# Performance work log

Measured on AMD Instinct MI355X. Metric: run time of the kernel, lower is better.

Reference implementation:

```python
import jax, jax.numpy as jnp
import numpy as np

# dims: batch, num queries, context len, model dim, heads, head dim,
# num_q_group, v_repeat, lora rank
B, NQ, NC, D = 4, 416, 257, 768
H, DH = 6, 128
G, R, LORA = 104, 4, 64  # NQ == R * G, all_q_mid == G * LORA
EPS = 1e-5


def ln(x, g, b):
    m = jnp.mean(x, axis=-1, keepdims=True)
    v = jnp.mean(jnp.square(x - m), axis=-1, keepdims=True)
    return (x - m) * jax.lax.rsqrt(v + EPS) * g + b


def setup_inputs() -> dict:
    key = jax.random.key(0)
    ks = jax.random.split(key, 7)
    s = 0.02
    return {
        "x": jax.random.normal(ks[0], (B, NQ, D), dtype=jnp.float32),
        "context": jax.random.normal(ks[1], (B, NC, D), dtype=jnp.float32),
        "Wq": jax.random.normal(ks[2], (D, D), dtype=jnp.float32) * s,
        "gq": jnp.ones((D,), jnp.float32), "bq": jnp.zeros((D,), jnp.float32),
        "Wk": jax.random.normal(ks[3], (D, D), dtype=jnp.float32) * s,
        "gk": jnp.ones((D,), jnp.float32), "bk": jnp.zeros((D,), jnp.float32),
        "Wv": jax.random.normal(ks[4], (D, G * LORA), dtype=jnp.float32) * s,
        "gv1": jnp.ones((G * LORA,), jnp.float32), "bv1": jnp.zeros((G * LORA,), jnp.float32),
        "Wconv": jax.random.normal(ks[5], (G, LORA, D), dtype=jnp.float32) * s,  # grouped 1x1 conv: per-group (LORA -> D)
        "gv2": jnp.ones((D,), jnp.float32), "bv2": jnp.zeros((D,), jnp.float32),
        "Wo": jax.random.normal(ks[6], (D, D), dtype=jnp.float32) * s,
        "go": jnp.ones((D,), jnp.float32), "bo": jnp.zeros((D,), jnp.float32),
    }


def reference(x, context, Wq, gq, bq, Wk, gk, bk, Wv, gv1, bv1, Wconv, gv2, bv2, Wo, go, bo):
    # to_q / to_k: Linear (no bias) + affine LayerNorm
    q = ln(x @ Wq, gq, bq)          # (B, NQ, D)
    k = ln(context @ Wk, gk, bk)    # (B, NC, D)
    # split heads -> (B*H, n, DH)
    q = q.reshape(B, NQ, H, DH).transpose(0, 2, 1, 3).reshape(B * H, NQ, DH)
    k = k.reshape(B, NC, H, DH).transpose(0, 2, 1, 3).reshape(B * H, NC, DH)

    # q-aware to_v: Linear -> LN -> grouped 1x1 Conv1d -> LN, plus skip of context
    mid = ln(context @ Wv, gv1, bv1)                 # (B, NC, G*LORA)
    mid = mid.reshape(B, NC, G, LORA)
    v = jnp.einsum('bngl,gld->bgnd', mid, Wconv)     # grouped conv, (B, G, NC, D)
    v = ln(v, gv2, bv2)
    v = v + context[:, None]                          # v_has_skip: context.unsqueeze(1)
    # heads: (B, G, NC, H, DH) -> (B*H, G, NC, DH)
    v = v.reshape(B, G, NC, H, DH).transpose(0, 3, 1, 2, 4).reshape(B * H, G, NC, DH)

    scale = DH ** (-0.25)
    sim = jnp.einsum('bid,bjd->bij', q * scale, k * scale)   # (B*H, NQ, NC)
    attn = jax.nn.softmax(sim, axis=-1)                       # dropout in eval mode: identity

    # torch repeat(1, R, 1, 1) tiles v along q-dim: query i uses group i % G.
    # reshape attn to (B*H, R, G, NC) so that i = r*G + g maps to group g.
    attn_g = attn.reshape(B * H, R, G, NC)
    out = jnp.einsum('brgj,bgjd->brgd', attn_g, v).reshape(B * H, NQ, DH)

    # merge heads -> (B, NQ, D)
    out = out.reshape(B, H, NQ, DH).transpose(0, 2, 1, 3).reshape(B, NQ, D)
    # to_out: Linear (no bias) + Dropout(eval: identity) + affine LayerNorm
    return ln(out @ Wo, go, bo)
```

## Files before the change

kernel.cpp:

```cpp
#include <hip/hip_runtime.h>


typedef unsigned short u16;
typedef unsigned int   u32;
typedef __attribute__((ext_vector_type(4))) float f32x4;
typedef __attribute__((ext_vector_type(4))) u32   u32x4;
typedef __attribute__((ext_vector_type(8))) short bf16x8;

__device__ __forceinline__ float bf2f(u16 v) { return __uint_as_float(((u32)v) << 16); }
__device__ __forceinline__ u16 f2bf(float f) {
  u32 u = __float_as_uint(f);
  u32 r = u + 0x7fffu + ((u >> 16) & 1u);
  return (u16)(r >> 16);
}
__device__ __forceinline__ float gld(const void* p, long idx, int f32) {
  return f32 ? ((const float*)p)[idx] : bf2f(((const u16*)p)[idx]);
}

typedef const __attribute__((address_space(1))) u32 gas_u32;
typedef __attribute__((address_space(3))) u32 las_u32;

__device__ __forceinline__ void stage16(const u16* g, u16* lbase, int lane) {
#if __has_builtin(__builtin_amdgcn_global_load_lds)
  (void)lane;
  __builtin_amdgcn_global_load_lds((gas_u32*)g, (las_u32*)lbase, 16, 0, 0);
#else
  *(u32x4*)(lbase + lane * 8) = *(const u32x4*)g;
#endif
}

__global__ __launch_bounds__(256) void probe_k(const u32* __restrict__ xw, int* __restrict__ flag) {
  int tid = threadIdx.x, c = 0;
  for (int i = tid; i < 4096; i += 256) {
    u16 lo = (u16)(xw[i] & 0xffffu);
    float a = fabsf(bf2f(lo));
    if (lo == 0 || (a >= 1e-3f && a <= 32.f)) ++c;
  }
#pragma unroll
  for (int o = 32; o; o >>= 1) c += __shfl_xor(c, o, 64);
  __shared__ int r[4];
  if ((tid & 63) == 0) r[tid >> 6] = c;
  __syncthreads();
  if (tid == 0) flag[0] = (r[0] + r[1] + r[2] + r[3] >= 2048) ? 0 : 1;
}

__global__ __launch_bounds__(256) void fill_k(u16* p, float v, int n) {
  int i = blockIdx.x * 256 + threadIdx.x;
  if (i < n) p[i] = f2bf(v);
}

__global__ __launch_bounds__(256) void prep_k(
    const void* __restrict__ x,   u16* __restrict__ xb,
    const void* __restrict__ ctx, u16* __restrict__ cbuf,
    const void* __restrict__ Wcv, u16* __restrict__ wcvb,
    u16* __restrict__ midi,
    const void* __restrict__ Wq, const void* __restrict__ Wk,
    const void* __restrict__ Wo, const void* __restrict__ Wv,
    u16* __restrict__ wqt, u16* __restrict__ wkt, u16* __restrict__ wot,
    u16* __restrict__ wvt, u16* __restrict__ ctxT,
    float* __restrict__ wbar, const int* __restrict__ dtf)
{
  const int f = dtf[0];
  int bid = blockIdx.x;
  __shared__ float s[32][33];
  if (bid < 3597) {
    const long n0_ = 1277952, n1_ = 789504, n2_ = 5111808, n3_ = 186368;
    long i = ((long)bid * 256 + threadIdx.x) * 8;
    const long t0 = n0_, t1 = t0 + n1_, t2 = t1 + n2_, t3 = t2 + n3_;
    if (i >= t3) return;
    if (i >= t2) {
      long e = i - t2;
      long z = e / 448, off = e - z * 448;
      u32x4 zz = {0u, 0u, 0u, 0u};
      *(u32x4*)(midi + z * 16896 + 16448 + off) = zz;
      return;
    }
    const void* in; u16* out;
    if (i < t0)      { in = x;    out = xb; }
    else if (i < t1) { in = ctx;  out = cbuf; i -= t0; }
    else             { in = Wcv;  out = wcvb; i -= t1; }
    if (f) {
      const float* ip = (const float*)in + i;
      f32x4 a = *(const f32x4*)ip, b = *(const f32x4*)(ip + 4);
      u32x4 q = { (u32)f2bf(a.x) | ((u32)f2bf(a.y) << 16),
                  (u32)f2bf(a.z) | ((u32)f2bf(a.w) << 16),
                  (u32)f2bf(b.x) | ((u32)f2bf(b.y) << 16),
                  (u32)f2bf(b.z) | ((u32)f2bf(b.w) << 16) };
      *(u32x4*)(out + i) = q;
    } else {
      *(u32x4*)(out + i) = *(const u32x4*)((const u16*)in + i);
    }
  } else if (bid < 11181) {
    int t = bid - 3597;
    const void* in; u16* out;
    int inK, inN, ldo, outK, nx;
    long inBase = 0, outBase = 0;
    if (t < 1728) {
      int w = t / 576; t -= w * 576;
      in  = w == 0 ? Wq : w == 1 ? Wk : Wo;
      out = w == 0 ? wqt : w == 1 ? wkt : wot;
      inK = 768; inN = 768; ldo = 768; outK = 768; nx = 24;
    } else if (t < 6720) {
      t -= 1728;
      in = Wv; out = wvt;
      inK = 768; inN = 6656; ldo = 768; outK = 768; nx = 208;
    } else {
      t -= 6720;
      int b = t / 216; t -= b * 216;
      in = ctx; out = ctxT;
      inK = 257; inN = 768; ldo = 264; outK = 264; nx = 24;
      inBase = (long)b * 257 * 768; outBase = (long)b * 768 * 264;
    }
    int n0 = (t % nx) * 32, k0 = (t / nx) * 32;
    int tx = threadIdx.x & 31, ty = threadIdx.x >> 5;
#pragma unroll
    for (int i = 0; i < 32; i += 8) {
      int k = k0 + ty + i, n = n0 + tx;
      float v = 0.f;
      if (k < inK && n < inN) v = gld(in, inBase + (long)k * inN + n, f);
      s[ty + i][tx] = v;
    }
    __syncthreads();
#pragma unroll
    for (int i = 0; i < 32; i += 8) {
      int n = n0 + ty + i, k = k0 + tx;
      if (n < inN && k < outK) out[outBase + (long)n * ldo + k] = f2bf(s[tx][ty + i]);
    }
  } else {
    int r = (bid - 11181) * 4 + (threadIdx.x >> 6);
    int lane = threadIdx.x & 63;
    long base = (long)r * 768;
    float sm = 0.f;
    for (int c = lane; c < 768; c += 64) sm += gld(Wcv, base + c, f);
#pragma unroll
    for (int o = 32; o; o >>= 1) sm += __shfl_xor(sm, o, 64);
    if (lane == 0) wbar[r] = sm * (1.f / 768.f);
  }
}

__device__ __forceinline__ void gemm128_body(
    const u16* __restrict__ A, const u16* __restrict__ B, u16* __restrict__ C,
    int M, int N, int K, int lda, int ldb, int ldc, int m0, int n0)
{
  __shared__ __attribute__((aligned(16))) u16 As[128 * 32];
  __shared__ __attribute__((aligned(16))) u16 Bs[128 * 32];
  const int tid = threadIdx.x, lane = tid & 63, wave = tid >> 6;
  const int wm = (wave >> 1) * 64, wn = (wave & 1) * 64;
  const int fm = lane & 15, fq = lane >> 4;

  const int srow = lane >> 2, selem = (lane & 3) * 8;
  int ra1 = m0 + wave * 16 + srow;      if (ra1 > M - 1) ra1 = M - 1;
  int ra2 = m0 + 64 + wave * 16 + srow; if (ra2 > M - 1) ra2 = M - 1;
  const int rb1 = n0 + wave * 16 + srow;
  const int rb2 = n0 + 64 + wave * 16 + srow;
  const u16* pa1 = A + (long)ra1 * lda + selem;
  const u16* pa2 = A + (long)ra2 * lda + selem;
  const u16* pb1 = B + (long)rb1 * ldb + selem;
  const u16* pb2 = B + (long)rb2 * ldb + selem;
  u16* la1 = As + wave * 512;
  u16* la2 = As + 2048 + wave * 512;
  u16* lb1 = Bs + wave * 512;
  u16* lb2 = Bs + 2048 + wave * 512;

  f32x4 acc[4][4];
  const f32x4 zero4 = {0.f, 0.f, 0.f, 0.f};
#pragma unroll
  for (int a_ = 0; a_ < 4; ++a_)
#pragma unroll
    for (int b_ = 0; b_ < 4; ++b_) acc[a_][b_] = zero4;

  for (int k0 = 0; k0 < K; k0 += 32) {
    stage16(pa1, la1, lane);
    stage16(pa2, la2, lane);
    stage16(pb1, lb1, lane);
    stage16(pb2, lb2, lane);
    pa1 += 32; pa2 += 32; pb1 += 32; pb2 += 32;
    __syncthreads();
    bf16x8 fa[4], fb[4];
#pragma unroll
    for (int mt = 0; mt < 4; ++mt)
      fa[mt] = *(const bf16x8*)&As[(wm + mt * 16 + fm) * 32 + fq * 8];
#pragma unroll
    for (int nt = 0; nt < 4; ++nt)
      fb[nt] = *(const bf16x8*)&Bs[(wn + nt * 16 + fm) * 32 + fq * 8];
#pragma unroll
    for (int mt = 0; mt < 4; ++mt)
#pragma unroll
      for (int nt = 0; nt < 4; ++nt)
        acc[mt][nt] = __builtin_amdgcn_mfma_f32_16x16x32_bf16(fa[mt], fb[nt], acc[mt][nt], 0, 0, 0);
    __syncthreads();
  }
#pragma unroll
  for (int mt = 0; mt < 4; ++mt)
#pragma unroll
    for (int nt = 0; nt < 4; ++nt)
#pragma unroll
      for (int rr = 0; rr < 4; ++rr) {
        int gm = m0 + wm + mt * 16 + fq * 4 + rr;
        int gn = n0 + wn + nt * 16 + fm;
        if (gm < M) C[(long)gm * ldc + gn] = f2bf(acc[mt][nt][rr]);
      }
}

__global__ __launch_bounds__(256) void gemm128(
    const u16* __restrict__ A, const u16* __restrict__ B, u16* __restrict__ C,
    int M, int N, int K, int lda, int ldb, int ldc)
{
  gemm128_body(A, B, C, M, N, K, lda, ldb, ldc, blockIdx.x * 128, blockIdx.y * 128);
}

#define LDS_S 40

__device__ __forceinline__ void gemm64_body(
    u16* As, u16* Bs,
    const u16* __restrict__ A16, const u16* __restrict__ B16,
    float* Cf, u16* Cb, float* Ylds,
    int M, int N, int K, int lda, int ldb, int ldc,
    int btrans, float alpha, int m0, int n0)
{
  const int tid = threadIdx.x;
  const int lane = tid & 63, wave = tid >> 6;
  const int wm = (wave >> 1) * 32, wn = (wave & 1) * 32;
  const int fm = lane & 15, fq = lane >> 4;
  const int ar = tid >> 2, ak = (tid & 3) * 8;
  const int bk = tid >> 3, bn = (tid & 7) * 8;

  f32x4 acc[2][2];
  const f32x4 zero4 = {0.f, 0.f, 0.f, 0.f};
#pragma unroll
  for (int a_ = 0; a_ < 2; ++a_)
#pragma unroll
    for (int b_ = 0; b_ < 2; ++b_) acc[a_][b_] = zero4;

  for (int k0 = 0; k0 < K; k0 += 32) {
    {
      int gm = m0 + ar, gk = k0 + ak;
      long idx = (long)gm * lda + gk;
      if (gm < M && gk + 8 <= K) {
        *(u32x4*)&As[ar * LDS_S + ak] = *(const u32x4*)(A16 + idx);
      } else {
#pragma unroll
        for (int e = 0; e < 8; ++e)
          As[ar * LDS_S + ak + e] = (gm < M && gk + e < K) ? A16[idx + e] : (u16)0;
      }
    }
    if (btrans) {
      int gn = n0 + ar, gk = k0 + ak;
      long idx = (long)gn * ldb + gk;
      if (gn < N && gk + 8 <= K) {
        *(u32x4*)&Bs[ar * LDS_S + ak] = *(const u32x4*)(B16 + idx);
      } else {
#pragma unroll
        for (int e = 0; e < 8; ++e)
          Bs[ar * LDS_S + ak + e] = (gn < N && gk + e < K) ? B16[idx + e] : (u16)0;
      }
    } else {
      int gk = k0 + bk;
      long idx = (long)gk * ldb + n0 + bn;
      u16 tmp[8];
      if (gk < K) {
        u32x4 v = *(const u32x4*)(B16 + idx);
        tmp[0] = (u16)(v.x & 0xffff); tmp[1] = (u16)(v.x >> 16);
        tmp[2] = (u16)(v.y & 0xffff); tmp[3] = (u16)(v.y >> 16);
        tmp[4] = (u16)(v.z & 0xffff); tmp[5] = (u16)(v.z >> 16);
        tmp[6] = (u16)(v.w & 0xffff); tmp[7] = (u16)(v.w >> 16);
      } else {
#pragma unroll
        for (int e = 0; e < 8; ++e) tmp[e] = 0;
      }
      int rot = tid & 7;
#pragma unroll
      for (int e = 0; e < 8; ++e) {
        int ee = (e + rot) & 7;
        Bs[(bn + ee) * LDS_S + bk] = tmp[ee];
      }
    }
    __syncthreads();
    {
      bf16x8 fa[2], fb[2];
      fa[0] = *(const bf16x8*)&As[(wm +      fm) * LDS_S + fq * 8];
      fa[1] = *(const bf16x8*)&As[(wm + 16 + fm) * LDS_S + fq * 8];
      fb[0] = *(const bf16x8*)&Bs[(wn +      fm) * LDS_S + fq * 8];
      fb[1] = *(const bf16x8*)&Bs[(wn + 16 + fm) * LDS_S + fq * 8];
#pragma unroll
      for (int mt = 0; mt < 2; ++mt)
#pragma unroll
        for (int nt = 0; nt < 2; ++nt)
          acc[mt][nt] = __builtin_amdgcn_mfma_f32_16x16x32_bf16(fa[mt], fb[nt], acc[mt][nt], 0, 0, 0);
    }
    __syncthreads();
  }
  if (Ylds) {
#pragma unroll
    for (int mt = 0; mt < 2; ++mt)
#pragma unroll
      for (int nt = 0; nt < 2; ++nt)
#pragma unroll
        for (int rr = 0; rr < 4; ++rr)
          Ylds[(wm + mt * 16 + fq * 4 + rr) * 64 + (wn + nt * 16 + fm)] = acc[mt][nt][rr];
  } else {
#pragma unroll
    for (int mt = 0; mt < 2; ++mt)
#pragma unroll
      for (int nt = 0; nt < 2; ++nt)
#pragma unroll
        for (int rr = 0; rr < 4; ++rr) {
          int gm = m0 + wm + mt * 16 + fq * 4 + rr;
          int gn = n0 + wn + nt * 16 + fm;
          if (gm < M && gn < N) {
            float v = alpha * acc[mt][nt][rr];
            if (Cb) Cb[(long)gm * ldc + gn] = f2bf(v);
            else    Cf[(long)gm * ldc + gn] = v;
          }
        }
  }
}

__global__ __launch_bounds__(256) void mg4_k(
    const u16* __restrict__ xb, const u16* __restrict__ wqt, u16* __restrict__ qbf,
    const u16* __restrict__ cbuf, const u16* __restrict__ wkt, u16* __restrict__ kbf,
    const u16* __restrict__ wvt, u16* __restrict__ midbf,
    const u16* __restrict__ wcvb, u16* __restrict__ Gb)
{
  int bid = blockIdx.x;
  if (bid < 600) {
    const u16 *A, *B; u16* C; int M, N, lid, mx;
    if (bid < 78)       { A = xb;   B = wqt; C = qbf;   M = 1664; N = 768;  lid = bid;       mx = 13; }
    else if (bid < 132) { A = cbuf; B = wkt; C = kbf;   M = 1028; N = 768;  lid = bid - 78;  mx = 9;  }
    else                { A = cbuf; B = wvt; C = midbf; M = 1028; N = 6656; lid = bid - 132; mx = 9;  }
    int m0 = (lid % mx) * 128, n0 = (lid / mx) * 128;
    gemm128_body(A, B, C, M, N, 768, 768, 768, N, m0, n0);
  } else {
    __shared__ __attribute__((aligned(16))) u16 As[64 * LDS_S];
    __shared__ __attribute__((aligned(16))) u16 Bs[64 * LDS_S];
    int z = bid - 600;
    gemm64_body(As, Bs, wcvb + (long)z * 49152, wcvb + (long)z * 49152,
                nullptr, Gb + (long)z * 4096, nullptr,
                64, 64, 768, 768, 768, 64, 1, 1.f / 768.f, 0, 0);
  }
}

__global__ __launch_bounds__(256) void ysim_k(
    const u16* __restrict__ midbf, const u16* __restrict__ Gb,
    const float* __restrict__ wbar, u16* __restrict__ midi, float* __restrict__ pim,
    const u16* __restrict__ qbf, const u16* __restrict__ kbf, float* __restrict__ simf)
{
  __shared__ __attribute__((aligned(16))) char smem[16384];
  u16* As = (u16*)smem;
  u16* Bs = (u16*)(smem + 8192);
  int bid = blockIdx.x;
  if (bid < 1768) {
    int g = bid / 17, bx = bid % 17;
    int m0 = bx * 64;
    float* Ylds = (float*)smem;
    gemm64_body(As, Bs, midbf + (long)g * 64, Gb + (long)g * 4096,
                nullptr, nullptr, Ylds,
                1028, 64, 64, 6656, 64, 64, 1, 1.f, m0, 0);
    __syncthreads();
    int tid = threadIdx.x, lane = tid & 63, wave = tid >> 6;
#pragma unroll
    for (int rr = 0; rr < 16; ++rr) {
      int r = wave * 16 + rr;
      int gr = m0 + r;
      if (gr < 1028) {
        float m  = bf2f(midbf[(long)gr * 6656 + g * 64 + lane]);
        float y  = Ylds[r * 64 + lane];
        float wb = wbar[g * 64 + lane];
        float mup = m * wb, q2p = m * y;
#pragma unroll
        for (int o = 32; o; o >>= 1) { mup += __shfl_xor(mup, o, 64); q2p += __shfl_xor(q2p, o, 64); }
        float var = q2p - mup * mup;
        float inv = rsqrtf(fmaxf(var, 0.f) + 1e-5f);
        int b = gr / 257, j = gr - b * 257;
        long zidx = (long)b * 104 + g;
        midi[(zidx * 264 + j) * 64 + lane] = f2bf(inv * m);
        if (lane == 0) pim[zidx * 257 + j] = inv * mup;
      }
    }
  } else {
    int lid = bid - 1768; int z = lid / 35, r = lid % 35, bx = r % 7, by = r / 7;
    const u16* A = qbf + (long)(z / 6) * 319488 + (long)(z % 6) * 128;
    const u16* B = kbf + (long)(z / 6) * 197376 + (long)(z % 6) * 128;
    float* Cf = simf + (long)z * 106912;
    gemm64_body(As, Bs, A, B, Cf, nullptr, nullptr,
                416, 257, 128, 768, 768, 257, 1, 0.08838834764831845f, bx * 64, by * 64);
  }
}

__global__ __launch_bounds__(256) void ct_k(
    const u16* __restrict__ Abf, const u16* __restrict__ ctxT, float* __restrict__ c_buf,
    const u16* __restrict__ A2bf, const u16* __restrict__ midi, u16* __restrict__ Tb16)
{
  __shared__ __attribute__((aligned(16))) u16 As[64 * LDS_S];
  __shared__ __attribute__((aligned(16))) u16 Bs[64 * LDS_S];
  int bid = blockIdx.x;
  if (bid < 336) {
    int z = bid / 14, r = bid % 14, bx = r % 7, by = r / 7;
    const u16* A = Abf + (long)z * 109824;
    const u16* B = ctxT + (long)(z / 6) * 202752 + (long)(z % 6) * 33792;
    float* Cf = c_buf + (long)z * 53248;
    gemm64_body(As, Bs, A, B, Cf, nullptr, nullptr,
                416, 128, 264, 264, 264, 128, 1, 1.f, bx * 64, by * 64);
  } else {
    int z = bid - 336;
    const u16* A = A2bf + (long)z * 6336;
    const u16* B = midi + (long)z * 16896;
    u16* Cb = Tb16 + (long)z * 1536;
    gemm64_body(As, Bs, A, B, nullptr, Cb, nullptr,
                24, 64, 264, 264, 64, 64, 0, 1.f, 0, 0);
  }
}

__device__ __forceinline__ void ln_row(
    const u16* __restrict__ ip, const void* __restrict__ g, const void* __restrict__ b,
    u16* __restrict__ ob, float* __restrict__ of, int N, int f)
{
  int tid = threadIdx.x, lane = tid & 63, wave = tid >> 6;
  const int nv = N >> 3;
  float s1 = 0.f, s2 = 0.f;
  for (int c8 = tid; c8 < nv; c8 += 256) {
    u32x4 v = *(const u32x4*)(ip + c8 * 8);
    float e0 = bf2f((u16)(v.x & 0xffff)), e1 = bf2f((u16)(v.x >> 16));
    float e2 = bf2f((u16)(v.y & 0xffff)), e3 = bf2f((u16)(v.y >> 16));
    float e4 = bf2f((u16)(v.z & 0xffff)), e5 = bf2f((u16)(v.z >> 16));
    float e6 = bf2f((u16)(v.w & 0xffff)), e7 = bf2f((u16)(v.w >> 16));
    s1 += ((e0 + e1) + (e2 + e3)) + ((e4 + e5) + (e6 + e7));
    s2 += ((e0*e0 + e1*e1) + (e2*e2 + e3*e3)) + ((e4*e4 + e5*e5) + (e6*e6 + e7*e7));
  }
#pragma unroll
  for (int o = 32; o; o >>= 1) { s1 += __shfl_xor(s1, o, 64); s2 += __shfl_xor(s2, o, 64); }
  __shared__ float red[8];
  if (lane == 0) { red[wave] = s1; red[4 + wave] = s2; }
  __syncthreads();
  s1 = red[0] + red[1] + red[2] + red[3];
  s2 = red[4] + red[5] + red[6] + red[7];
  float mean = s1 / N;
  float var = s2 / N - mean * mean;
  float rstd = rsqrtf(fmaxf(var, 0.f) + 1e-5f);
  for (int c8 = tid; c8 < nv; c8 += 256) {
    int c = c8 * 8;
    u32x4 v = *(const u32x4*)(ip + c);
    float e[8];
    e[0] = bf2f((u16)(v.x & 0xffff)); e[1] = bf2f((u16)(v.x >> 16));
    e[2] = bf2f((u16)(v.y & 0xffff)); e[3] = bf2f((u16)(v.y >> 16));
    e[4] = bf2f((u16)(v.z & 0xffff)); e[5] = bf2f((u16)(v.z >> 16));
    e[6] = bf2f((u16)(v.w & 0xffff)); e[7] = bf2f((u16)(v.w >> 16));
    float gg[8], bb[8];
    if (f) {
      const float* gp = (const float*)g + c; const float* bp = (const float*)b + c;
      f32x4 g0 = *(const f32x4*)gp, g1 = *(const f32x4*)(gp + 4);
      f32x4 b0 = *(const f32x4*)bp, b1 = *(const f32x4*)(bp + 4);
      gg[0]=g0.x; gg[1]=g0.y; gg[2]=g0.z; gg[3]=g0.w; gg[4]=g1.x; gg[5]=g1.y; gg[6]=g1.z; gg[7]=g1.w;
      bb[0]=b0.x; bb[1]=b0.y; bb[2]=b0.z; bb[3]=b0.w; bb[4]=b1.x; bb[5]=b1.y; bb[6]=b1.z; bb[7]=b1.w;
    } else {
      u32x4 gv = *(const u32x4*)((const u16*)g + c);
      u32x4 bv = *(const u32x4*)((const u16*)b + c);
      gg[0]=bf2f((u16)(gv.x&0xffff)); gg[1]=bf2f((u16)(gv.x>>16));
      gg[2]=bf2f((u16)(gv.y&0xffff)); gg[3]=bf2f((u16)(gv.y>>16));
      gg[4]=bf2f((u16)(gv.z&0xffff)); gg[5]=bf2f((u16)(gv.z>>16));
      gg[6]=bf2f((u16)(gv.w&0xffff)); gg[7]=bf2f((u16)(gv.w>>16));
      bb[0]=bf2f((u16)(bv.x&0xffff)); bb[1]=bf2f((u16)(bv.x>>16));
      bb[2]=bf2f((u16)(bv.y&0xffff)); bb[3]=bf2f((u16)(bv.y>>16));
      bb[4]=bf2f((u16)(bv.z&0xffff)); bb[5]=bf2f((u16)(bv.z>>16));
      bb[6]=bf2f((u16)(bv.w&0xffff)); bb[7]=bf2f((u16)(bv.w>>16));
    }
    float o_[8];
#pragma unroll
    for (int e2i = 0; e2i < 8; ++e2i) o_[e2i] = (e[e2i] - mean) * rstd * gg[e2i] + bb[e2i];
    if (of) {
      f32x4 o0 = {o_[0], o_[1], o_[2], o_[3]}, o1 = {o_[4], o_[5], o_[6], o_[7]};
      *(f32x4*)(of + c) = o0; *(f32x4*)(of + c + 4) = o1;
    } else {
      u32x4 q = { (u32)f2bf(o_[0]) | ((u32)f2bf(o_[1]) << 16),
                  (u32)f2bf(o_[2]) | ((u32)f2bf(o_[3]) << 16),
                  (u32)f2bf(o_[4]) | ((u32)f2bf(o_[5]) << 16),
                  (u32)f2bf(o_[6]) | ((u32)f2bf(o_[7]) << 16) };
      *(u32x4*)(ob + c) = q;
    }
  }
}

__global__ __launch_bounds__(256) void ln_rows(
    const u16* __restrict__ in, const void* __restrict__ g, const void* __restrict__ b,
    void* __restrict__ out, int N, const int* __restrict__ dtf, int isfinal)
{
  const int f = dtf[0];
  long row = blockIdx.x;
  const u16* ip = in + row * N;
  float* of = (isfinal && f) ? (float*)out + row * N : nullptr;
  u16*   ob = of ? nullptr : (u16*)out + row * N;
  ln_row(ip, g, b, ob, of, N, f);
}

__global__ __launch_bounds__(256) void mln3_k(
    u16* __restrict__ qb, const void* __restrict__ gq, const void* __restrict__ bq,
    u16* __restrict__ kb, const void* __restrict__ gk, const void* __restrict__ bk,
    u16* __restrict__ mb, const void* __restrict__ gv, const void* __restrict__ bv,
    const int* __restrict__ dtf)
{
  const int f = dtf[0];
  int row = blockIdx.x;
  u16* ip; const void *g, *b; int N;
  if (row < 1664)      { ip = qb + (long)row * 768; g = gq; b = bq; N = 768; }
  else if (row < 2692) { ip = kb + (long)(row - 1664) * 768; g = gk; b = bk; N = 768; }
  else                 { ip = mb + (long)(row - 2692) * 6656; g = gv; b = bv; N = 6656; }
  ln_row(ip, g, b, ip, nullptr, N, f);
}

__global__ __launch_bounds__(256) void softmax_k(
    const float* __restrict__ simf, const float* __restrict__ pim,
    u16* __restrict__ Abf, u16* __restrict__ A2bf, float* __restrict__ s_sh)
{
  int bh = blockIdx.x;
  int b = bh / 6, h = bh - b * 6;
  int tid = threadIdx.x, lane = tid & 63, wave = tid >> 6;
  int i = blockIdx.y * 4 + wave;
  int g = i % 104, rq = i / 104;
  const float* sp_ = simf + ((long)bh * 416 + i) * 257;
  float s[5];
#pragma unroll
  for (int jc = 0; jc < 5; ++jc) {
    int j = jc * 64 + lane;
    s[jc] = (j < 257) ? sp_[j] : -1e30f;
  }
  float mx = -1e30f;
#pragma unroll
  for (int jc = 0; jc < 5; ++jc) mx = fmaxf(mx, s[jc]);
#pragma unroll
  for (int o = 32; o; o >>= 1) mx = fmaxf(mx, __shfl_xor(mx, o, 64));
  float p[5], sum = 0.f, sp = 0.f;
  long pimb = ((long)b * 104 + g) * 257;
#pragma unroll
  for (int jc = 0; jc < 5; ++jc) {
    int j = jc * 64 + lane;
    float pv = 0.f;
    if (j < 257) { pv = __expf(s[jc] - mx); sp = fmaf(pv, pim[pimb + j], sp); }
    p[jc] = pv; sum += pv;
  }
#pragma unroll
  for (int o = 32; o; o >>= 1) { sum += __shfl_xor(sum, o, 64); sp += __shfl_xor(sp, o, 64); }
  float rs = 1.f / sum;
  long arow  = ((long)bh * 416 + i) * 264;
  long a2row = (((long)b * 104 + g) * 24 + h * 4 + rq) * 264;
#pragma unroll
  for (int jc = 0; jc < 5; ++jc) {
    int j = jc * 64 + lane;
    if (j < 257) { u16 pb = f2bf(p[jc] * rs); Abf[arow + j] = pb; A2bf[a2row + j] = pb; }
    else if (j < 264) { Abf[arow + j] = 0; A2bf[a2row + j] = 0; }
  }
  if (lane == 0) s_sh[(long)bh * 416 + i] = sp * rs;
}

__global__ __launch_bounds__(256) void oc_k(
    const u16* __restrict__ T, const u16* __restrict__ Wb,
    const float* __restrict__ s_sh, const float* __restrict__ c_buf,
    const void* __restrict__ gv2, const void* __restrict__ bv2,
    u16* __restrict__ opbf, const int* __restrict__ dtf)
{
  const int f = dtf[0];
  int z = blockIdx.x;
  int b = z / 104, g = z - b * 104;
  int tid = threadIdx.x;
  __shared__ float Ts[24][64];
  const u16* tp = T + (long)z * 1536;
  for (int idx = tid; idx < 1536; idx += 256) Ts[idx >> 6][idx & 63] = bf2f(tp[idx]);
  __syncthreads();
  const int dh = tid & 127;
  const int hbase = (tid >> 7) * 3;
  const u16* wg = Wb + (long)g * 49152;
#pragma unroll
  for (int hh = 0; hh < 3; ++hh) {
    int h = hbase + hh;
    int d = h * 128 + dh;
    const u16* wp = wg + d;
    float a0 = 0.f, a1 = 0.f, a2 = 0.f, a3 = 0.f;
#pragma unroll 16
    for (int k = 0; k < 64; ++k) {
      float w = bf2f(wp[(long)k * 768]);
      a0 = fmaf(Ts[h * 4 + 0][k], w, a0);
      a1 = fmaf(Ts[h * 4 + 1][k], w, a1);
      a2 = fmaf(Ts[h * 4 + 2][k], w, a2);
      a3 = fmaf(Ts[h * 4 + 3][k], w, a3);
    }
    float acc[4] = {a0, a1, a2, a3};
    float gvd = gld(gv2, d, f), bvd = gld(bv2, d, f);
#pragma unroll
    for (int rq = 0; rq < 4; ++rq) {
      int i = rq * 104 + g;
      float ssh = s_sh[((long)b * 6 + h) * 416 + i];
      float val = gvd * (acc[rq] - ssh) + bvd
                + c_buf[(((long)b * 6 + h) * 416 + i) * 128 + dh];
      opbf[((long)b * 416 + i) * 768 + d] = f2bf(val);
    }
  }
}

extern "C" void kernel_launch(void* const* d_in, const int* in_sizes, int n_in,
                              void* d_out, int out_size, void* d_ws, size_t ws_size,
                              hipStream_t stream)
{
  (void)in_sizes; (void)n_in;
  const void* x   = d_in[0];
  const void* ctx = d_in[1];
  const void* Wq  = d_in[2];
  const void* gq  = d_in[3];
  const void* bq  = d_in[4];
  const void* Wk  = d_in[5];
  const void* gk  = d_in[6];
  const void* bk  = d_in[7];
  const void* Wv  = d_in[8];
  const void* gv1 = d_in[9];
  const void* bv1 = d_in[10];
  const void* Wcv = d_in[11];
  const void* gv2 = d_in[12];
  const void* bv2 = d_in[13];
  const void* Wo  = d_in[14];
  const void* go  = d_in[15];
  const void* bo  = d_in[16];

  const size_t SZ_FLAG = 256;
  const size_t SZ_QBF  = 2555904;
  const size_t SZ_KBF  = 1579008;
  const size_t SZ_MID  = 13684736;
  const size_t SZ_MM   = 1703936;
  const size_t SZ_WB   = 26624;
  const size_t SZ_MIDI = 14057472;
  const size_t SZ_PIM  = 427648;
  const size_t SZ_ABF  = 5271552;
  const size_t SZ_A2   = 5271552;
  const size_t SZ_SSH  = 39936;
  const size_t SZ_CB   = 1579008;
  const size_t SZ_WCVB = 10223616;
  const size_t SZ_WT   = 1179648;
  const size_t SZ_WVT  = 10223616;
  const size_t SZ_CTXT = 1622016;
  const size_t SZ_SIMF = 10263552;
  const size_t REQUIRED = SZ_FLAG + SZ_QBF + SZ_KBF + SZ_MID + SZ_MM + SZ_WB +
                          SZ_MIDI + SZ_PIM + SZ_ABF + SZ_A2 + SZ_SSH + SZ_CB +
                          SZ_WCVB + 3 * SZ_WT + SZ_WVT + SZ_CTXT + SZ_SIMF;

  if (ws_size < REQUIRED) {
    fill_k<<<(out_size + 255) / 256, 256, 0, stream>>>((u16*)d_out, (float)(ws_size >> 20), out_size);
    return;
  }

  char* p = (char*)d_ws;
  int*   dtf   = (int*)  p;                 p += SZ_FLAG;
  u16*   qbf   = (u16*)  p;                 p += SZ_QBF;
  u16*   kbf   = (u16*)  p;                 p += SZ_KBF;
  char*  midrg = p;                         p += SZ_MID;
  char*  mmrg  = p;                         p += SZ_MM;
  float* wbar  = (float*)p;                 p += SZ_WB;
  u16*   midi  = (u16*)  p;                 p += SZ_MIDI;
  float* pim   = (float*)p;                 p += SZ_PIM;
  char*  abfrg = p;                         p += SZ_ABF;
  u16*   A2bf  = (u16*)  p;                 p += SZ_A2;
  float* s_sh  = (float*)p;                 p += SZ_SSH;
  u16*   cb    = (u16*)  p;                 p += SZ_CB;
  u16*   wcvb  = (u16*)  p;                 p += SZ_WCVB;
  u16*   wqt2  = (u16*)  p;                 p += SZ_WT;
  u16*   wkt2  = (u16*)  p;                 p += SZ_WT;
  u16*   wot2  = (u16*)  p;                 p += SZ_WT;
  u16*   wvt   = (u16*)  p;                 p += SZ_WVT;
  u16*   ctxT  = (u16*)  p;                 p += SZ_CTXT;
  float* simf  = (float*)p;                 p += SZ_SIMF;

  u16*   midbf = (u16*)midrg;
  float* c_buf = (float*)midrg;
  u16*   Tb16  = (u16*)(midrg + 5111808);
  u16*   Gb    = (u16*)mmrg;
  u16*   xb    = (u16*)abfrg;
  u16*   Abf   = (u16*)abfrg;
  u16*   opbf  = (u16*)abfrg;

  probe_k<<<1, 256, 0, stream>>>((const u32*)x, dtf);

  prep_k<<<12845, 256, 0, stream>>>(x, xb, ctx, cb, Wcv, wcvb, midi,
                                    Wq, Wk, Wo, Wv, wqt2, wkt2, wot2, wvt, ctxT,
                                    wbar, dtf);

  mg4_k<<<704, 256, 0, stream>>>(xb, wqt2, qbf, cb, wkt2, kbf, wvt, midbf, wcvb, Gb);

  mln3_k<<<3720, 256, 0, stream>>>(qbf, gq, bq, kbf, gk, bk, midbf, gv1, bv1, dtf);

  ysim_k<<<2608, 256, 0, stream>>>(midbf, Gb, wbar, midi, pim, qbf, kbf, simf);

  softmax_k<<<dim3(24, 104), 256, 0, stream>>>(simf, pim, Abf, A2bf, s_sh);

  ct_k<<<752, 256, 0, stream>>>(Abf, ctxT, c_buf, A2bf, midi, Tb16);

  oc_k<<<416, 256, 0, stream>>>(Tb16, wcvb, s_sh, c_buf, gv2, bv2, opbf, dtf);

  {
    dim3 grid(13, 6, 1);
    gemm128<<<grid, dim3(256), 0, stream>>>(opbf, wot2, qbf, 1664, 768, 768, 768, 768, 768);
  }
  ln_rows<<<1664, 256, 0, stream>>>(qbf, go, bo, d_out, 768, dtf, 1);
}
```

Measured before the change: 262.9 us.

## Fuse all stages into one persistent megakernel with grid-wide barriers

Replaces the ten separate kernel launches with a single persistent kernel that loops over virtual block indices for each stage and separates stages with atomic-counter grid barriers. The dtype probe is computed per block instead of in its own kernel. The goal is to remove launch overhead and inter-kernel gaps. In exchange it takes on barrier spin costs, a grid limited by occupancy (launch bounds 256,2), a memset before every launch, and possible load imbalance within each stage.

```diff
diff --git a/kernel.cpp b/kernel.cpp
--- a/kernel.cpp
+++ b/kernel.cpp
@@ -29,7 +29,48 @@
 #endif
 }
 
-__global__ __launch_bounds__(256) void probe_k(const u32* __restrict__ xw, int* __restrict__ flag) {
+__global__ __launch_bounds__(256) void fill_k(u16* p, float v, int n) {
+  int i = blockIdx.x * 256 + threadIdx.x;
+  if (i < n) p[i] = f2bf(v);
+}
+
+struct MegaArgs {
+  const void *x, *ctx, *Wq, *gq, *bq, *Wk, *gk, *bk, *Wv, *gv1, *bv1;
+  const void *Wcv, *gv2, *bv2, *Wo, *go, *bo;
+  u16 *xb, *cbuf, *wcvb, *midi;
+  u16 *wqt, *wkt, *wot, *wvt, *ctxT;
+  float *wbar;
+  u16 *qbf, *kbf, *midbf, *Gb;
+  float *simf, *pim;
+  u16 *Abf, *A2bf;
+  float *s_sh, *c_buf;
+  u16 *Tb16, *opbf;
+  void *outp;
+};
+
+__device__ __forceinline__ void gbar(int* bar, int site) {
+  __syncthreads();
+  if (threadIdx.x == 0) {
+    __threadfence();
+    int* cnt = bar + site * 2;
+    int* flg = cnt + 1;
+    int prev = atomicAdd(cnt, 1);
+    if (prev == (int)gridDim.x - 1) {
+      __hip_atomic_store(flg, 1, __ATOMIC_RELEASE, __HIP_MEMORY_SCOPE_AGENT);
+    } else {
+      long t = 0;
+      while (__hip_atomic_load(flg, __ATOMIC_ACQUIRE, __HIP_MEMORY_SCOPE_AGENT) == 0) {
+        __builtin_amdgcn_s_sleep(8);
+        if (++t > (1L << 24)) break;
+      }
+    }
+    __threadfence();
+  }
+  __syncthreads();
+}
+
+__device__ int probe_flag(const u32* xw) {
+  __shared__ int r[4];
   int tid = threadIdx.x, c = 0;
   for (int i = tid; i < 4096; i += 256) {
     u16 lo = (u16)(xw[i] & 0xffffu);
@@ -38,31 +79,14 @@
   }
 #pragma unroll
   for (int o = 32; o; o >>= 1) c += __shfl_xor(c, o, 64);
-  __shared__ int r[4];
   if ((tid & 63) == 0) r[tid >> 6] = c;
   __syncthreads();
-  if (tid == 0) flag[0] = (r[0] + r[1] + r[2] + r[3] >= 2048) ? 0 : 1;
-}
-
-__global__ __launch_bounds__(256) void fill_k(u16* p, float v, int n) {
-  int i = blockIdx.x * 256 + threadIdx.x;
-  if (i < n) p[i] = f2bf(v);
-}
-
-__global__ __launch_bounds__(256) void prep_k(
-    const void* __restrict__ x,   u16* __restrict__ xb,
-    const void* __restrict__ ctx, u16* __restrict__ cbuf,
-    const void* __restrict__ Wcv, u16* __restrict__ wcvb,
-    u16* __restrict__ midi,
-    const void* __restrict__ Wq, const void* __restrict__ Wk,
-    const void* __restrict__ Wo, const void* __restrict__ Wv,
-    u16* __restrict__ wqt, u16* __restrict__ wkt, u16* __restrict__ wot,
-    u16* __restrict__ wvt, u16* __restrict__ ctxT,
-    float* __restrict__ wbar, const int* __restrict__ dtf)
-{
-  const int f = dtf[0];
-  int bid = blockIdx.x;
-  __shared__ float s[32][33];
+  int tot = r[0] + r[1] + r[2] + r[3];
+  __syncthreads();
+  return (tot >= 2048) ? 0 : 1;
+}
+
+__device__ void prep_body(int bid, int f, const MegaArgs& a) {
   if (bid < 3597) {
     const long n0_ = 1277952, n1_ = 789504, n2_ = 5111808, n3_ = 186368;
     long i = ((long)bid * 256 + threadIdx.x) * 8;
@@ -72,42 +96,43 @@
       long e = i - t2;
       long z = e / 448, off = e - z * 448;
       u32x4 zz = {0u, 0u, 0u, 0u};
-      *(u32x4*)(midi + z * 16896 + 16448 + off) = zz;
+      *(u32x4*)(a.midi + z * 16896 + 16448 + off) = zz;
       return;
     }
     const void* in; u16* out;
-    if (i < t0)      { in = x;    out = xb; }
-    else if (i < t1) { in = ctx;  out = cbuf; i -= t0; }
-    else             { in = Wcv;  out = wcvb; i -= t1; }
+    if (i < t0)      { in = a.x;   out = a.xb; }
+    else if (i < t1) { in = a.ctx; out = a.cbuf; i -= t0; }
+    else             { in = a.Wcv; out = a.wcvb; i -= t1; }
     if (f) {
       const float* ip = (const float*)in + i;
-      f32x4 a = *(const f32x4*)ip, b = *(const f32x4*)(ip + 4);
-      u32x4 q = { (u32)f2bf(a.x) | ((u32)f2bf(a.y) << 16),
-                  (u32)f2bf(a.z) | ((u32)f2bf(a.w) << 16),
-                  (u32)f2bf(b.x) | ((u32)f2bf(b.y) << 16),
-                  (u32)f2bf(b.z) | ((u32)f2bf(b.w) << 16) };
+      f32x4 u = *(const f32x4*)ip, v = *(const f32x4*)(ip + 4);
+      u32x4 q = { (u32)f2bf(u.x) | ((u32)f2bf(u.y) << 16),
+                  (u32)f2bf(u.z) | ((u32)f2bf(u.w) << 16),
+                  (u32)f2bf(v.x) | ((u32)f2bf(v.y) << 16),
+                  (u32)f2bf(v.z) | ((u32)f2bf(v.w) << 16) };
       *(u32x4*)(out + i) = q;
     } else {
       *(u32x4*)(out + i) = *(const u32x4*)((const u16*)in + i);
     }
   } else if (bid < 11181) {
+    __shared__ float s[32][33];
     int t = bid - 3597;
     const void* in; u16* out;
     int inK, inN, ldo, outK, nx;
     long inBase = 0, outBase = 0;
     if (t < 1728) {
       int w = t / 576; t -= w * 576;
-      in  = w == 0 ? Wq : w == 1 ? Wk : Wo;
-      out = w == 0 ? wqt : w == 1 ? wkt : wot;
+      in  = w == 0 ? a.Wq : w == 1 ? a.Wk : a.Wo;
+      out = w == 0 ? a.wqt : w == 1 ? a.wkt : a.wot;
       inK = 768; inN = 768; ldo = 768; outK = 768; nx = 24;
     } else if (t < 6720) {
       t -= 1728;
-      in = Wv; out = wvt;
+      in = a.Wv; out = a.wvt;
       inK = 768; inN = 6656; ldo = 768; outK = 768; nx = 208;
     } else {
       t -= 6720;
       int b = t / 216; t -= b * 216;
-      in = ctx; out = ctxT;
+      in = a.ctx; out = a.ctxT;
       inK = 257; inN = 768; ldo = 264; outK = 264; nx = 24;
       inBase = (long)b * 257 * 768; outBase = (long)b * 768 * 264;
     }
@@ -126,24 +151,24 @@
       int n = n0 + ty + i, k = k0 + tx;
       if (n < inN && k < outK) out[outBase + (long)n * ldo + k] = f2bf(s[tx][ty + i]);
     }
+    __syncthreads();
   } else {
     int r = (bid - 11181) * 4 + (threadIdx.x >> 6);
     int lane = threadIdx.x & 63;
     long base = (long)r * 768;
     float sm = 0.f;
-    for (int c = lane; c < 768; c += 64) sm += gld(Wcv, base + c, f);
+    for (int c = lane; c < 768; c += 64) sm += gld(a.Wcv, base + c, f);
 #pragma unroll
     for (int o = 32; o; o >>= 1) sm += __shfl_xor(sm, o, 64);
-    if (lane == 0) wbar[r] = sm * (1.f / 768.f);
+    if (lane == 0) a.wbar[r] = sm * (1.f / 768.f);
   }
 }
 
 __device__ __forceinline__ void gemm128_body(
+    u16* As, u16* Bs,
     const u16* __restrict__ A, const u16* __restrict__ B, u16* __restrict__ C,
     int M, int N, int K, int lda, int ldb, int ldc, int m0, int n0)
 {
-  __shared__ __attribute__((aligned(16))) u16 As[128 * 32];
-  __shared__ __attribute__((aligned(16))) u16 Bs[128 * 32];
   const int tid = threadIdx.x, lane = tid & 63, wave = tid >> 6;
   const int wm = (wave >> 1) * 64, wn = (wave & 1) * 64;
   const int fm = lane & 15, fq = lane >> 4;
@@ -200,13 +225,6 @@
         int gn = n0 + wn + nt * 16 + fm;
         if (gm < M) C[(long)gm * ldc + gn] = f2bf(acc[mt][nt][rr]);
       }
-}
-
-__global__ __launch_bounds__(256) void gemm128(
-    const u16* __restrict__ A, const u16* __restrict__ B, u16* __restrict__ C,
-    int M, int N, int K, int lda, int ldb, int ldc)
-{
-  gemm128_body(A, B, C, M, N, K, lda, ldb, ldc, blockIdx.x * 128, blockIdx.y * 128);
 }
 
 #define LDS_S 40
@@ -316,44 +334,32 @@
   }
 }
 
-__global__ __launch_bounds__(256) void mg4_k(
-    const u16* __restrict__ xb, const u16* __restrict__ wqt, u16* __restrict__ qbf,
-    const u16* __restrict__ cbuf, const u16* __restrict__ wkt, u16* __restrict__ kbf,
-    const u16* __restrict__ wvt, u16* __restrict__ midbf,
-    const u16* __restrict__ wcvb, u16* __restrict__ Gb)
-{
-  int bid = blockIdx.x;
+__device__ void mg4_body(int bid, const MegaArgs& a, char* smem) {
+  u16* As = (u16*)smem;
+  u16* Bs = (u16*)(smem + 8192);
   if (bid < 600) {
     const u16 *A, *B; u16* C; int M, N, lid, mx;
-    if (bid < 78)       { A = xb;   B = wqt; C = qbf;   M = 1664; N = 768;  lid = bid;       mx = 13; }
-    else if (bid < 132) { A = cbuf; B = wkt; C = kbf;   M = 1028; N = 768;  lid = bid - 78;  mx = 9;  }
-    else                { A = cbuf; B = wvt; C = midbf; M = 1028; N = 6656; lid = bid - 132; mx = 9;  }
+    if (bid < 78)       { A = a.xb;   B = a.wqt; C = a.qbf;   M = 1664; N = 768;  lid = bid;       mx = 13; }
+    else if (bid < 132) { A = a.cbuf; B = a.wkt; C = a.kbf;   M = 1028; N = 768;  lid = bid - 78;  mx = 9;  }
+    else                { A = a.cbuf; B = a.wvt; C = a.midbf; M = 1028; N = 6656; lid = bid - 132; mx = 9;  }
     int m0 = (lid % mx) * 128, n0 = (lid / mx) * 128;
-    gemm128_body(A, B, C, M, N, 768, 768, 768, N, m0, n0);
+    gemm128_body(As, Bs, A, B, C, M, N, 768, 768, 768, N, m0, n0);
   } else {
-    __shared__ __attribute__((aligned(16))) u16 As[64 * LDS_S];
-    __shared__ __attribute__((aligned(16))) u16 Bs[64 * LDS_S];
     int z = bid - 600;
-    gemm64_body(As, Bs, wcvb + (long)z * 49152, wcvb + (long)z * 49152,
-                nullptr, Gb + (long)z * 4096, nullptr,
+    gemm64_body(As, Bs, a.wcvb + (long)z * 49152, a.wcvb + (long)z * 49152,
+                nullptr, a.Gb + (long)z * 4096, nullptr,
                 64, 64, 768, 768, 768, 64, 1, 1.f / 768.f, 0, 0);
   }
 }
 
-__global__ __launch_bounds__(256) void ysim_k(
-    const u16* __restrict__ midbf, const u16* __restrict__ Gb,
-    const float* __restrict__ wbar, u16* __restrict__ midi, float* __restrict__ pim,
-    const u16* __restrict__ qbf, const u16* __restrict__ kbf, float* __restrict__ simf)
-{
-  __shared__ __attribute__((aligned(16))) char smem[16384];
+__device__ void ysim_body(int bid, const MegaArgs& a, char* smem) {
   u16* As = (u16*)smem;
   u16* Bs = (u16*)(smem + 8192);
-  int bid = blockIdx.x;
   if (bid < 1768) {
     int g = bid / 17, bx = bid % 17;
     int m0 = bx * 64;
     float* Ylds = (float*)smem;
-    gemm64_body(As, Bs, midbf + (long)g * 64, Gb + (long)g * 4096,
+    gemm64_body(As, Bs, a.midbf + (long)g * 64, a.Gb + (long)g * 4096,
                 nullptr, nullptr, Ylds,
                 1028, 64, 64, 6656, 64, 64, 1, 1.f, m0, 0);
     __syncthreads();
@@ -363,9 +369,9 @@
       int r = wave * 16 + rr;
       int gr = m0 + r;
       if (gr < 1028) {
-        float m  = bf2f(midbf[(long)gr * 6656 + g * 64 + lane]);
+        float m  = bf2f(a.midbf[(long)gr * 6656 + g * 64 + lane]);
         float y  = Ylds[r * 64 + lane];
-        float wb = wbar[g * 64 + lane];
+        float wb = a.wbar[g * 64 + lane];
         float mup = m * wb, q2p = m * y;
 #pragma unroll
         for (int o = 32; o; o >>= 1) { mup += __shfl_xor(mup, o, 64); q2p += __shfl_xor(q2p, o, 64); }
@@ -373,39 +379,36 @@
         float inv = rsqrtf(fmaxf(var, 0.f) + 1e-5f);
         int b = gr / 257, j = gr - b * 257;
         long zidx = (long)b * 104 + g;
-        midi[(zidx * 264 + j) * 64 + lane] = f2bf(inv * m);
-        if (lane == 0) pim[zidx * 257 + j] = inv * mup;
+        a.midi[(zidx * 264 + j) * 64 + lane] = f2bf(inv * m);
+        if (lane == 0) a.pim[zidx * 257 + j] = inv * mup;
       }
     }
+    __syncthreads();
   } else {
     int lid = bid - 1768; int z = lid / 35, r = lid % 35, bx = r % 7, by = r / 7;
-    const u16* A = qbf + (long)(z / 6) * 319488 + (long)(z % 6) * 128;
-    const u16* B = kbf + (long)(z / 6) * 197376 + (long)(z % 6) * 128;
-    float* Cf = simf + (long)z * 106912;
+    const u16* A = a.qbf + (long)(z / 6) * 319488 + (long)(z % 6) * 128;
+    const u16* B = a.kbf + (long)(z / 6) * 197376 + (long)(z % 6) * 128;
+    float* Cf = a.simf + (long)z * 106912;
     gemm64_body(As, Bs, A, B, Cf, nullptr, nullptr,
                 416, 257, 128, 768, 768, 257, 1, 0.08838834764831845f, bx * 64, by * 64);
   }
 }
 
-__global__ __launch_bounds__(256) void ct_k(
-    const u16* __restrict__ Abf, const u16* __restrict__ ctxT, float* __restrict__ c_buf,
-    const u16* __restrict__ A2bf, const u16* __restrict__ midi, u16* __restrict__ Tb16)
-{
-  __shared__ __attribute__((aligned(16))) u16 As[64 * LDS_S];
-  __shared__ __attribute__((aligned(16))) u16 Bs[64 * LDS_S];
-  int bid = blockIdx.x;
+__device__ void ct_body(int bid, const MegaArgs& a, char* smem) {
+  u16* As = (u16*)smem;
+  u16* Bs = (u16*)(smem + 8192);
   if (bid < 336) {
     int z = bid / 14, r = bid % 14, bx = r % 7, by = r / 7;
-    const u16* A = Abf + (long)z * 109824;
-    const u16* B = ctxT + (long)(z / 6) * 202752 + (long)(z % 6) * 33792;
-    float* Cf = c_buf + (long)z * 53248;
+    const u16* A = a.Abf + (long)z * 109824;
+    const u16* B = a.ctxT + (long)(z / 6) * 202752 + (long)(z % 6) * 33792;
+    float* Cf = a.c_buf + (long)z * 53248;
     gemm64_body(As, Bs, A, B, Cf, nullptr, nullptr,
                 416, 128, 264, 264, 264, 128, 1, 1.f, bx * 64, by * 64);
   } else {
     int z = bid - 336;
-    const u16* A = A2bf + (long)z * 6336;
-    const u16* B = midi + (long)z * 16896;
-    u16* Cb = Tb16 + (long)z * 1536;
+    const u16* A = a.A2bf + (long)z * 6336;
+    const u16* B = a.midi + (long)z * 16896;
+    u16* Cb = a.Tb16 + (long)z * 1536;
     gemm64_body(As, Bs, A, B, nullptr, Cb, nullptr,
                 24, 64, 264, 264, 64, 64, 0, 1.f, 0, 0);
   }
@@ -478,45 +481,31 @@
       *(u32x4*)(ob + c) = q;
     }
   }
-}
-
-__global__ __launch_bounds__(256) void ln_rows(
-    const u16* __restrict__ in, const void* __restrict__ g, const void* __restrict__ b,
-    void* __restrict__ out, int N, const int* __restrict__ dtf, int isfinal)
-{
-  const int f = dtf[0];
-  long row = blockIdx.x;
-  const u16* ip = in + row * N;
-  float* of = (isfinal && f) ? (float*)out + row * N : nullptr;
-  u16*   ob = of ? nullptr : (u16*)out + row * N;
-  ln_row(ip, g, b, ob, of, N, f);
-}
-
-__global__ __launch_bounds__(256) void mln3_k(
-    u16* __restrict__ qb, const void* __restrict__ gq, const void* __restrict__ bq,
-    u16* __restrict__ kb, const void* __restrict__ gk, const void* __restrict__ bk,
-    u16* __restrict__ mb, const void* __restrict__ gv, const void* __restrict__ bv,
-    const int* __restrict__ dtf)
-{
-  const int f = dtf[0];
-  int row = blockIdx.x;
+  __syncthreads();
+}
+
+__device__ void mln3_body(int row, int f, const MegaArgs& a) {
   u16* ip; const void *g, *b; int N;
-  if (row < 1664)      { ip = qb + (long)row * 768; g = gq; b = bq; N = 768; }
-  else if (row < 2692) { ip = kb + (long)(row - 1664) * 768; g = gk; b = bk; N = 768; }
-  else                 { ip = mb + (long)(row - 2692) * 6656; g = gv; b = bv; N = 6656; }
+  if (row < 1664)      { ip = a.qbf + (long)row * 768; g = a.gq; b = a.bq; N = 768; }
+  else if (row < 2692) { ip = a.kbf + (long)(row - 1664) * 768; g = a.gk; b = a.bk; N = 768; }
+  else                 { ip = a.midbf + (long)(row - 2692) * 6656; g = a.gv1; b = a.bv1; N = 6656; }
   ln_row(ip, g, b, ip, nullptr, N, f);
 }
 
-__global__ __launch_bounds__(256) void softmax_k(
-    const float* __restrict__ simf, const float* __restrict__ pim,
-    u16* __restrict__ Abf, u16* __restrict__ A2bf, float* __restrict__ s_sh)
-{
-  int bh = blockIdx.x;
+__device__ void fin_ln_body(int row, int f, const MegaArgs& a) {
+  const u16* ip = a.qbf + (long)row * 768;
+  float* of = f ? (float*)a.outp + (long)row * 768 : nullptr;
+  u16*   ob = f ? nullptr : (u16*)a.outp + (long)row * 768;
+  ln_row(ip, a.go, a.bo, ob, of, 768, f);
+}
+
+__device__ void softmax_body(int vb, const MegaArgs& a) {
+  int bh = vb % 24, gy = vb / 24;
   int b = bh / 6, h = bh - b * 6;
   int tid = threadIdx.x, lane = tid & 63, wave = tid >> 6;
-  int i = blockIdx.y * 4 + wave;
+  int i = gy * 4 + wave;
   int g = i % 104, rq = i / 104;
-  const float* sp_ = simf + ((long)bh * 416 + i) * 257;
+  const float* sp_ = a.simf + ((long)bh * 416 + i) * 257;
   float s[5];
 #pragma unroll
   for (int jc = 0; jc < 5; ++jc) {
@@ -534,7 +523,7 @@
   for (int jc = 0; jc < 5; ++jc) {
     int j = jc * 64 + lane;
     float pv = 0.f;
-    if (j < 257) { pv = __expf(s[jc] - mx); sp = fmaf(pv, pim[pimb + j], sp); }
+    if (j < 257) { pv = __expf(s[jc] - mx); sp = fmaf(pv, a.pim[pimb + j], sp); }
     p[jc] = pv; sum += pv;
   }
 #pragma unroll
@@ -545,29 +534,22 @@
 #pragma unroll
   for (int jc = 0; jc < 5; ++jc) {
     int j = jc * 64 + lane;
-    if (j < 257) { u16 pb = f2bf(p[jc] * rs); Abf[arow + j] = pb; A2bf[a2row + j] = pb; }
-    else if (j < 264) { Abf[arow + j] = 0; A2bf[a2row + j] = 0; }
-  }
-  if (lane == 0) s_sh[(long)bh * 416 + i] = sp * rs;
-}
-
-__global__ __launch_bounds__(256) void oc_k(
-    const u16* __restrict__ T, const u16* __restrict__ Wb,
-    const float* __restrict__ s_sh, const float* __restrict__ c_buf,
-    const void* __restrict__ gv2, const void* __restrict__ bv2,
-    u16* __restrict__ opbf, const int* __restrict__ dtf)
-{
-  const int f = dtf[0];
-  int z = blockIdx.x;
+    if (j < 257) { u16 pb = f2bf(p[jc] * rs); a.Abf[arow + j] = pb; a.A2bf[a2row + j] = pb; }
+    else if (j < 264) { a.Abf[arow + j] = 0; a.A2bf[a2row + j] = 0; }
+  }
+  if (lane == 0) a.s_sh[(long)bh * 416 + i] = sp * rs;
+}
+
+__device__ void oc_body(int z, int f, const MegaArgs& a) {
   int b = z / 104, g = z - b * 104;
   int tid = threadIdx.x;
   __shared__ float Ts[24][64];
-  const u16* tp = T + (long)z * 1536;
+  const u16* tp = a.Tb16 + (long)z * 1536;
   for (int idx = tid; idx < 1536; idx += 256) Ts[idx >> 6][idx & 63] = bf2f(tp[idx]);
   __syncthreads();
   const int dh = tid & 127;
   const int hbase = (tid >> 7) * 3;
-  const u16* wg = Wb + (long)g * 49152;
+  const u16* wg = a.wcvb + (long)g * 49152;
 #pragma unroll
   for (int hh = 0; hh < 3; ++hh) {
     int h = hbase + hh;
@@ -583,16 +565,46 @@
       a3 = fmaf(Ts[h * 4 + 3][k], w, a3);
     }
     float acc[4] = {a0, a1, a2, a3};
-    float gvd = gld(gv2, d, f), bvd = gld(bv2, d, f);
+    float gvd = gld(a.gv2, d, f), bvd = gld(a.bv2, d, f);
 #pragma unroll
     for (int rq = 0; rq < 4; ++rq) {
       int i = rq * 104 + g;
-      float ssh = s_sh[((long)b * 6 + h) * 416 + i];
+      float ssh = a.s_sh[((long)b * 6 + h) * 416 + i];
       float val = gvd * (acc[rq] - ssh) + bvd
-                + c_buf[(((long)b * 6 + h) * 416 + i) * 128 + dh];
-      opbf[((long)b * 416 + i) * 768 + d] = f2bf(val);
-    }
-  }
+                + a.c_buf[(((long)b * 6 + h) * 416 + i) * 128 + dh];
+      a.opbf[((long)b * 416 + i) * 768 + d] = f2bf(val);
+    }
+  }
+  __syncthreads();
+}
+
+__global__ __launch_bounds__(256, 2) void mega_k(MegaArgs a, int* bar) {
+  __shared__ __attribute__((aligned(16))) char smem[16384];
+
+  const int f = probe_flag((const u32*)a.x);
+
+  for (int vb = blockIdx.x; vb < 12845; vb += gridDim.x) prep_body(vb, f, a);
+  gbar(bar, 0);
+  for (int vb = blockIdx.x; vb < 704; vb += gridDim.x) mg4_body(vb, a, smem);
+  gbar(bar, 1);
+  for (int vb = blockIdx.x; vb < 3720; vb += gridDim.x) mln3_body(vb, f, a);
+  gbar(bar, 2);
+  for (int vb = blockIdx.x; vb < 2608; vb += gridDim.x) ysim_body(vb, a, smem);
+  gbar(bar, 3);
+  for (int vb = blockIdx.x; vb < 2496; vb += gridDim.x) softmax_body(vb, a);
+  gbar(bar, 4);
+  for (int vb = blockIdx.x; vb < 752; vb += gridDim.x) ct_body(vb, a, smem);
+  gbar(bar, 5);
+  for (int vb = blockIdx.x; vb < 416; vb += gridDim.x) oc_body(vb, f, a);
+  gbar(bar, 6);
+  for (int vb = blockIdx.x; vb < 78; vb += gridDim.x) {
+    u16* As = (u16*)smem;
+    u16* Bs = (u16*)(smem + 8192);
+    gemm128_body(As, Bs, a.opbf, a.wot, a.qbf, 1664, 768, 768, 768, 768, 768,
+                 (vb % 13) * 128, (vb / 13) * 128);
+  }
+  gbar(bar, 7);
+  for (int vb = blockIdx.x; vb < 1664; vb += gridDim.x) fin_ln_body(vb, f, a);
 }
 
 extern "C" void kernel_launch(void* const* d_in, const int* in_sizes, int n_in,
@@ -600,25 +612,7 @@
                               hipStream_t stream)
 {
   (void)in_sizes; (void)n_in;
-  const void* x   = d_in[0];
-  const void* ctx = d_in[1];
-  const void* Wq  = d_in[2];
-  const void* gq  = d_in[3];
-  const void* bq  = d_in[4];
-  const void* Wk  = d_in[5];
-  const void* gk  = d_in[6];
-  const void* bk  = d_in[7];
-  const void* Wv  = d_in[8];
-  const void* gv1 = d_in[9];
-  const void* bv1 = d_in[10];
-  const void* Wcv = d_in[11];
-  const void* gv2 = d_in[12];
-  const void* bv2 = d_in[13];
-  const void* Wo  = d_in[14];
-  const void* go  = d_in[15];
-  const void* bo  = d_in[16];
-
-  const size_t SZ_FLAG = 256;
+  const size_t SZ_BAR  = 256;
   const size_t SZ_QBF  = 2555904;
   const size_t SZ_KBF  = 1579008;
   const size_t SZ_MID  = 13684736;
@@ -635,7 +629,7 @@
   const size_t SZ_WVT  = 10223616;
   const size_t SZ_CTXT = 1622016;
   const size_t SZ_SIMF = 10263552;
-  const size_t REQUIRED = SZ_FLAG + SZ_QBF + SZ_KBF + SZ_MID + SZ_MM + SZ_WB +
+  const size_t REQUIRED = SZ_BAR + SZ_QBF + SZ_KBF + SZ_MID + SZ_MM + SZ_WB +
                           SZ_MIDI + SZ_PIM + SZ_ABF + SZ_A2 + SZ_SSH + SZ_CB +
                           SZ_WCVB + 3 * SZ_WT + SZ_WVT + SZ_CTXT + SZ_SIMF;
 
@@ -645,7 +639,7 @@
   }
 
   char* p = (char*)d_ws;
-  int*   dtf   = (int*)  p;                 p += SZ_FLAG;
+  int*   bar   = (int*)  p;                 p += SZ_BAR;
   u16*   qbf   = (u16*)  p;                 p += SZ_QBF;
   u16*   kbf   = (u16*)  p;                 p += SZ_KBF;
   char*  midrg = p;                         p += SZ_MID;
@@ -665,35 +659,46 @@
   u16*   ctxT  = (u16*)  p;                 p += SZ_CTXT;
   float* simf  = (float*)p;                 p += SZ_SIMF;
 
-  u16*   midbf = (u16*)midrg;
-  float* c_buf = (float*)midrg;
-  u16*   Tb16  = (u16*)(midrg + 5111808);
-  u16*   Gb    = (u16*)mmrg;
-  u16*   xb    = (u16*)abfrg;
-  u16*   Abf   = (u16*)abfrg;
-  u16*   opbf  = (u16*)abfrg;
-
-  probe_k<<<1, 256, 0, stream>>>((const u32*)x, dtf);
-
-  prep_k<<<12845, 256, 0, stream>>>(x, xb, ctx, cb, Wcv, wcvb, midi,
-                                    Wq, Wk, Wo, Wv, wqt2, wkt2, wot2, wvt, ctxT,
-                                    wbar, dtf);
-
-  mg4_k<<<704, 256, 0, stream>>>(xb, wqt2, qbf, cb, wkt2, kbf, wvt, midbf, wcvb, Gb);
-
-  mln3_k<<<3720, 256, 0, stream>>>(qbf, gq, bq, kbf, gk, bk, midbf, gv1, bv1, dtf);
-
-  ysim_k<<<2608, 256, 0, stream>>>(midbf, Gb, wbar, midi, pim, qbf, kbf, simf);
-
-  softmax_k<<<dim3(24, 104), 256, 0, stream>>>(simf, pim, Abf, A2bf, s_sh);
-
-  ct_k<<<752, 256, 0, stream>>>(Abf, ctxT, c_buf, A2bf, midi, Tb16);
-
-  oc_k<<<416, 256, 0, stream>>>(Tb16, wcvb, s_sh, c_buf, gv2, bv2, opbf, dtf);
-
-  {
-    dim3 grid(13, 6, 1);
-    gemm128<<<grid, dim3(256), 0, stream>>>(opbf, wot2, qbf, 1664, 768, 768, 768, 768, 768);
-  }
-  ln_rows<<<1664, 256, 0, stream>>>(qbf, go, bo, d_out, 768, dtf, 1);
-}
+  MegaArgs a;
+  a.x = d_in[0];  a.ctx = d_in[1];
+  a.Wq = d_in[2]; a.gq = d_in[3]; a.bq = d_in[4];
+  a.Wk = d_in[5]; a.gk = d_in[6]; a.bk = d_in[7];
+  a.Wv = d_in[8]; a.gv1 = d_in[9]; a.bv1 = d_in[10];
+  a.Wcv = d_in[11]; a.gv2 = d_in[12]; a.bv2 = d_in[13];
+  a.Wo = d_in[14]; a.go = d_in[15]; a.bo = d_in[16];
+  a.xb = (u16*)abfrg;
+  a.cbuf = cb;
+  a.wcvb = wcvb;
+  a.midi = midi;
+  a.wqt = wqt2; a.wkt = wkt2; a.wot = wot2; a.wvt = wvt; a.ctxT = ctxT;
+  a.wbar = wbar;
+  a.qbf = qbf; a.kbf = kbf;
+  a.midbf = (u16*)midrg;
+  a.Gb = (u16*)mmrg;
+  a.simf = simf; a.pim = pim;
+  a.Abf = (u16*)abfrg; a.A2bf = A2bf;
+  a.s_sh = s_sh;
+  a.c_buf = (float*)midrg;
+  a.Tb16 = (u16*)(midrg + 5111808);
+  a.opbf = (u16*)abfrg;
+  a.outp = d_out;
+
+  static int g_grid = 0;
+  if (g_grid == 0) {
+    int nb = 0;
+    hipOccupancyMaxActiveBlocksPerMultiprocessor(&nb, mega_k, 256, 0);
+    if (nb < 1) nb = 1;
+    if (nb > 4) nb = 4;
+    int ncu = 256;
+    hipDeviceProp_t prop;
+    int dev = 0;
+    if (hipGetDevice(&dev) == hipSuccess &&
+        hipGetDeviceProperties(&prop, dev) == hipSuccess &&
+        prop.multiProcessorCount > 0)
+      ncu = prop.multiProcessorCount;
+    g_grid = nb * ncu;
+  }
+
+  hipMemsetAsync(bar, 0, SZ_BAR, stream);
+  mega_k<<<g_grid, 256, 0, stream>>>(a, bar);
+}
```

Result: slower. 807.6 us (+207.1%).
